# Performance work log

Hardware: AMD Instinct MI355X
Metric: run time of the kernel (lower is better)

The kernel has to match this reference:

```python
import jax, jax.numpy as jnp
import numpy as np

N_NODES = 100000
N_EDGES = 1600000
IN_DIM = 128
HID = 128
OUT = 128
NUM_GRAPHS = 2048


def setup_inputs() -> dict:
    key = jax.random.key(0)
    ks = jax.random.split(key, 10)
    x = jax.random.normal(ks[0], (N_NODES, IN_DIM), dtype=jnp.float32)
    edge_index = jax.random.randint(ks[1], (2, N_EDGES), 0, N_NODES, dtype=jnp.int32)
    graph_index = jnp.sort(jax.random.randint(ks[2], (N_NODES,), 0, NUM_GRAPHS, dtype=jnp.int32))
    def glorot(k, fi, fo):
        lim = jnp.sqrt(6.0 / (fi + fo)).astype(jnp.float32)
        return jax.random.uniform(k, (fi, fo), jnp.float32, -lim, lim)
    return {
        "x": x,
        "edge_index": edge_index,
        "graph_index": graph_index,
        "num_graphs": NUM_GRAPHS,
        "W1": glorot(ks[3], IN_DIM, HID), "b1": jnp.zeros((HID,), jnp.float32),
        "W2": glorot(ks[4], HID, HID),    "b2": jnp.zeros((HID,), jnp.float32),
        "W3": glorot(ks[5], HID, OUT),    "b3": jnp.zeros((OUT,), jnp.float32),
    }


def _gcn_layer(x, src, dst, norm, W, b, n_nodes):
    # transform first (cheap GEMM), then normalized gather-scatter aggregation
    h = x @ W                              # [N, F]
    msg = h[src] * norm[:, None]           # [E+N, F] gather + scale
    out = jax.ops.segment_sum(msg, dst, num_segments=n_nodes)  # scatter-add
    return out + b


def reference(x, edge_index, graph_index, num_graphs, W1, b1, W2, b2, W3, b3):
    n = x.shape[0]
    # add self-loops (PyG GCNConv default)
    loops = jnp.arange(n, dtype=edge_index.dtype)
    src = jnp.concatenate([edge_index[0], loops])
    dst = jnp.concatenate([edge_index[1], loops])
    # symmetric normalization D^-1/2 (A+I) D^-1/2, degree = in-degree incl. self-loop
    deg = jax.ops.segment_sum(jnp.ones_like(src, dtype=x.dtype), dst, num_segments=n)
    dinv = jax.lax.rsqrt(jnp.maximum(deg, 1.0))
    norm = dinv[src] * dinv[dst]
    # 3 conv layers + ReLU (dropout = identity at inference)
    h = jax.nn.relu(_gcn_layer(x, src, dst, norm, W1, b1, n))
    h = jax.nn.relu(_gcn_layer(h, src, dst, norm, W2, b2, n))
    h = jax.nn.relu(_gcn_layer(h, src, dst, norm, W3, b3, n))
    # global mean / max pooling per graph
    gsum = jax.ops.segment_sum(h, graph_index, num_segments=num_graphs)
    cnt = jax.ops.segment_sum(jnp.ones((n,), h.dtype), graph_index, num_segments=num_graphs)
    gmean = gsum / jnp.maximum(cnt, 1.0)[:, None]
    gmax = jax.ops.segment_max(h, graph_index, num_segments=num_graphs)
    return jnp.concatenate([gmean, gmax], axis=-1)
```

## Files before the change

### kernel.cpp

```cpp
#include <hip/hip_runtime.h>
#include <hip/hip_bf16.h>
#include <stdint.h>

#define N_NODES   100000
#define N_EDGES   1600000
#define FDIM      128
#define NUM_GR    2048
#define CSR_CAP   64

#define NBKT      391
#define BKT_CAP   4864
#define TILE      4096
#define LBIN_CAP  32
#define LBIN_STR  33

typedef __attribute__((ext_vector_type(8))) short short8;
typedef __attribute__((ext_vector_type(4))) float f32x4;

__device__ __forceinline__ uint32_t pk2(float a, float b) {
    __hip_bfloat16 x = __float2bfloat16(a), y = __float2bfloat16(b);
    uint16_t ux = *reinterpret_cast<uint16_t*>(&x);
    uint16_t uy = *reinterpret_cast<uint16_t*>(&y);
    return (uint32_t)ux | ((uint32_t)uy << 16);
}

__device__ __forceinline__ float bflo(uint32_t u) { return __uint_as_float(u << 16); }
__device__ __forceinline__ float bfhi(uint32_t u) { return __uint_as_float(u & 0xFFFF0000u); }


__global__ __launch_bounds__(256) void k_bucket_wprep(
        const int* __restrict__ src, const int* __restrict__ dst,
        int* __restrict__ bkt_cnt, int* __restrict__ bkt, int E, int gA,
        const float* __restrict__ W1, const float* __restrict__ W2,
        const float* __restrict__ W3, __hip_bfloat16* __restrict__ wt) {
    int b = blockIdx.x;
    if (b >= gA) {
        int idx = (b - gA) * 256 + threadIdx.x;
        int l = idx >> 14, rem = idx & 16383, c = rem >> 7, k = rem & 127;
        const float* W = (l == 0) ? W1 : ((l == 1) ? W2 : W3);
        wt[idx] = __float2bfloat16(W[k * FDIM + c]);
        return;
    }

    __shared__ int binCnt[NBKT];
    __shared__ int binBase[NBKT];
    __shared__ int bins[NBKT * LBIN_STR];

    for (int i = threadIdx.x; i < NBKT; i += 256) binCnt[i] = 0;
    __syncthreads();

    int e0 = b * TILE;
    int e1 = min(E, e0 + TILE);
    for (int e = e0 + threadIdx.x; e < e1; e += 256) {
        int s = src[e];
        int d = dst[e];
        int bi = d >> 8;
        int rec = ((d & 255) << 17) | s;
        int pos = atomicAdd(&binCnt[bi], 1);
        if (pos < LBIN_CAP) {
            bins[bi * LBIN_STR + pos] = rec;
        } else {
            int gp = atomicAdd(&bkt_cnt[bi], 1);
            if (gp < BKT_CAP) bkt[bi * BKT_CAP + gp] = rec;
        }
    }
    __syncthreads();

    for (int i = threadIdx.x; i < NBKT; i += 256) {
        int c = min(binCnt[i], LBIN_CAP);
        binBase[i] = (c > 0) ? atomicAdd(&bkt_cnt[i], c) : 0;
    }
    __syncthreads();

    for (int i = threadIdx.x; i < NBKT * LBIN_CAP; i += 256) {
        int bi = i / LBIN_CAP, sl = i - bi * LBIN_CAP;
        if (sl < min(binCnt[bi], LBIN_CAP)) {
            int gp = binBase[bi] + sl;
            if (gp < BKT_CAP) bkt[bi * BKT_CAP + gp] = bins[bi * LBIN_STR + sl];
        }
    }
}


__global__ __launch_bounds__(256) void k_csr(const int* __restrict__ bkt_cnt,
                                             const int* __restrict__ bkt,
                                             int* __restrict__ cnt,
                                             float* __restrict__ dinv,
                                             int* __restrict__ csr, int n) {
    __shared__ int lc[256];
    __shared__ int cur[256];
    int b = blockIdx.x;
    int tid = threadIdx.x;
    lc[tid] = 0;
    cur[tid] = 0;
    __syncthreads();

    int len = min(bkt_cnt[b], BKT_CAP);
    const int* recs = bkt + b * BKT_CAP;

    for (int i = tid; i < len; i += 256)
        atomicAdd(&lc[(recs[i] >> 17) & 255], 1);
    __syncthreads();

    int v = (b << 8) + tid;
    if (v < n) {
        int c = lc[tid];
        cnt[v] = c;
        dinv[v] = rsqrtf((float)(c + 1));
    }

    for (int i = tid; i < len; i += 256) {
        int rec = recs[i];
        int dl = (rec >> 17) & 255;
        int pos = atomicAdd(&cur[dl], 1);
        if (pos < CSR_CAP)
            csr[(((size_t)(b << 8) + dl) << 6) + pos] = rec & 0x1FFFF;
    }
}


template<bool AF32>
__global__ __launch_bounds__(256) void k_gemm(const void* __restrict__ Ap,
                                              const __hip_bfloat16* __restrict__ Wt,
                                              const float* __restrict__ dinv,
                                              __hip_bfloat16* __restrict__ C, int n) {
    __shared__ uint32_t lds[2 * 128 * 64];
    uint32_t* Atl = lds;
    uint32_t* Wtl = lds + 128 * 64;

    const int tid = threadIdx.x;
    const int rowBase = blockIdx.x * 128;

    if constexpr (AF32) {
        const float* A = (const float*)Ap;
        for (int it = 0; it < 16; ++it) {
            int g = it * 256 + tid;
            int r = g >> 5;
            int seg = g & 31;
            float4 v = make_float4(0.f, 0.f, 0.f, 0.f);
            if (rowBase + r < n) v = *(const float4*)&A[(size_t)(rowBase + r) * FDIM + seg * 4];
            int gg = seg >> 1;
            int word = r * 64 + (((gg ^ (r & 7)) << 2) | ((seg & 1) << 1));
            uint2 pv;
            pv.x = pk2(v.x, v.y);
            pv.y = pk2(v.z, v.w);
            *(uint2*)&Atl[word] = pv;
        }
    } else {
        const uint4* A4 = (const uint4*)Ap;
        for (int it = 0; it < 8; ++it) {
            int g = it * 256 + tid;
            int r = g >> 4;
            int seg = g & 15;
            uint4 v = make_uint4(0, 0, 0, 0);
            if (rowBase + r < n) v = A4[((size_t)rowBase + r) * 16 + seg];
            int word = r * 64 + ((seg ^ (r & 7)) << 2);
            *(uint4*)&Atl[word] = v;
        }
    }
    for (int it = 0; it < 8; ++it) {
        int g = it * 256 + tid;
        int r = g >> 4;
        int seg = g & 15;
        uint4 v = *(const uint4*)&Wt[(size_t)r * FDIM + seg * 8];
        int word = r * 64 + ((seg ^ (r & 7)) << 2);
        *(uint4*)&Wtl[word] = v;
    }
    __syncthreads();

    const int w = tid >> 6;
    const int lane = tid & 63;
    const int r = lane & 15;
    const int q = lane >> 4;

    f32x4 acc[8][2] = {};

#pragma unroll
    for (int kk = 0; kk < 4; ++kk) {
        int gr = ((kk * 4 + q) ^ (r & 7)) << 2;
        short8 a0 = *(const short8*)&Atl[(w * 32 + r) * 64 + gr];
        short8 a1 = *(const short8*)&Atl[(w * 32 + 16 + r) * 64 + gr];
#pragma unroll
        for (int m = 0; m < 8; ++m) {
            short8 bw = *(const short8*)&Wtl[(m * 16 + r) * 64 + gr];
            acc[m][0] = __builtin_amdgcn_mfma_f32_16x16x32_bf16(bw, a0, acc[m][0], 0, 0, 0);
            acc[m][1] = __builtin_amdgcn_mfma_f32_16x16x32_bf16(bw, a1, acc[m][1], 0, 0, 0);
        }
    }

#pragma unroll
    for (int nt = 0; nt < 2; ++nt) {
        int node = rowBase + w * 32 + nt * 16 + r;
        if (node < n) {
            float dv = dinv[node];
#pragma unroll
            for (int m = 0; m < 8; ++m) {
                f32x4 v = acc[m][nt];
                uint2 pv;
                pv.x = pk2(v[0] * dv, v[1] * dv);
                pv.y = pk2(v[2] * dv, v[3] * dv);
                *(uint2*)&C[(size_t)node * FDIM + m * 16 + q * 4] = pv;
            }
        }
    }
}


__global__ __launch_bounds__(256) void k_agg(const __hip_bfloat16* __restrict__ T,
                                             const int* __restrict__ cnt,
                                             const int* __restrict__ csr,
                                             const float* __restrict__ dinv,
                                             const float* __restrict__ bias,
                                             uint32_t* __restrict__ Hb,
                                             int n) {
    int wid = (blockIdx.x * 256 + threadIdx.x) >> 6;
    int lane = threadIdx.x & 63;
    if (wid >= n) return;
    int v = wid;
    int half = lane >> 5;
    int sub  = lane & 31;

    const uint2* Tu2 = (const uint2*)T;

    uint2 su = Tu2[(size_t)v * 32 + sub];
    float a0, a1, a2, a3;
    if (half == 0) { a0 = bflo(su.x); a1 = bfhi(su.x); a2 = bflo(su.y); a3 = bfhi(su.y); }
    else           { a0 = a1 = a2 = a3 = 0.f; }

    int cv = min(cnt[v], CSR_CAP);

    int sidx = (lane < cv) ? csr[((size_t)v << 6) + lane] : n;

    int mr = (cv + 15) & ~15;
    for (int j = 0; j < mr; j += 16) {
        uint2 gg[8];
#pragma unroll
        for (int t = 0; t < 8; ++t) {
            int it = __shfl(sidx, j + 2 * t + half, 64);
            gg[t] = Tu2[(size_t)it * 32 + sub];
        }
#pragma unroll
        for (int t = 0; t < 8; ++t) {
            a0 += bflo(gg[t].x);
            a1 += bfhi(gg[t].x);
            a2 += bflo(gg[t].y);
            a3 += bfhi(gg[t].y);
        }
    }

    float p0 = __shfl(a0, lane ^ 32, 64);
    float p1 = __shfl(a1, lane ^ 32, 64);
    float p2 = __shfl(a2, lane ^ 32, 64);
    float p3 = __shfl(a3, lane ^ 32, 64);
    a0 += p0; a1 += p1; a2 += p2; a3 += p3;

    if (half == 0) {
        float dv = dinv[v];
        float4 bb = *(const float4*)&bias[sub * 4];
        a0 = fmaxf(fmaf(dv, a0, bb.x), 0.f);
        a1 = fmaxf(fmaf(dv, a1, bb.y), 0.f);
        a2 = fmaxf(fmaf(dv, a2, bb.z), 0.f);
        a3 = fmaxf(fmaf(dv, a3, bb.w), 0.f);
        uint2 pv;
        pv.x = pk2(a0, a1);
        pv.y = pk2(a2, a3);
        *(uint2*)&Hb[(size_t)v * 64 + sub * 2] = pv;
    }
}


__device__ __forceinline__ int lower_bound_dev(const int* a, int n, int key) {
    int lo = 0, hi = n;
    while (lo < hi) {
        int m = (lo + hi) >> 1;
        if (a[m] < key) lo = m + 1; else hi = m;
    }
    return lo;
}

__global__ __launch_bounds__(64) void k_pool2(const uint32_t* __restrict__ Hb,
                                              const int* __restrict__ gidx,
                                              float* __restrict__ out, int n) {
    int g = blockIdx.x;
    int lane = threadIdx.x;

    int lo = lower_bound_dev(gidx, n, g);
    int hi = lower_bound_dev(gidx, n, g + 1);

    float s0 = 0.f, s1 = 0.f, m0 = 0.f, m1 = 0.f;
    for (int v = lo; v < hi; ++v) {
        uint32_t u = Hb[(size_t)v * 64 + lane];
        float x0 = bflo(u), x1 = bfhi(u);
        s0 += x0; s1 += x1;
        m0 = fmaxf(m0, x0); m1 = fmaxf(m1, x1);
    }
    float inv = 1.f / (float)max(hi - lo, 1);
    float* og = out + (size_t)g * 2 * FDIM;
    og[lane * 2]     = s0 * inv;
    og[lane * 2 + 1] = s1 * inv;
    og[FDIM + lane * 2]     = m0;
    og[FDIM + lane * 2 + 1] = m1;
}


extern "C" void kernel_launch(void* const* d_in, const int* in_sizes, int n_in,
                              void* d_out, int out_size, void* d_ws, size_t ws_size,
                              hipStream_t stream) {
    const float* x    = (const float*)d_in[0];
    const int*   ei   = (const int*)d_in[1];
    const int*   gidx = (const int*)d_in[2];
    const float* W1 = (const float*)d_in[4];
    const float* b1 = (const float*)d_in[5];
    const float* W2 = (const float*)d_in[6];
    const float* b2 = (const float*)d_in[7];
    const float* W3 = (const float*)d_in[8];
    const float* b3 = (const float*)d_in[9];
    float* out = (float*)d_out;

    const int N = N_NODES, E = N_EDGES;
    const int* src = ei;
    const int* dst = ei + E;

    char* ws = (char*)d_ws;
    size_t o = 0;
    auto alloc = [&](size_t bytes) { size_t r = o; o += (bytes + 255) & ~(size_t)255; return r; };
    size_t o_bktcnt = alloc((size_t)NBKT * 4);
    size_t o_bkt    = alloc((size_t)NBKT * BKT_CAP * 4);
    size_t o_cnt    = alloc((size_t)N * 4);
    size_t o_dinv   = alloc((size_t)N * 4);
    size_t o_csr    = alloc((size_t)NBKT * 256 * CSR_CAP * 4);
    size_t o_wt     = alloc((size_t)3 * FDIM * FDIM * 2);
    size_t o_t      = alloc((size_t)(N + 1) * FDIM * 2);
    size_t o_h      = alloc((size_t)N * FDIM * 2);

    int*   bkt_cnt = (int*)(ws + o_bktcnt);
    int*   bkt     = (int*)(ws + o_bkt);
    int*   cnt     = (int*)(ws + o_cnt);
    float* dinv    = (float*)(ws + o_dinv);
    int*   csr     = (int*)(ws + o_csr);
    __hip_bfloat16* wtbuf = (__hip_bfloat16*)(ws + o_wt);
    __hip_bfloat16* tbuf  = (__hip_bfloat16*)(ws + o_t);
    __hip_bfloat16* hb16  = (__hip_bfloat16*)(ws + o_h);

    hipMemsetAsync(bkt_cnt, 0, (size_t)NBKT * 4, stream);
    hipMemsetAsync(tbuf + (size_t)N * FDIM, 0, FDIM * 2, stream);

    const int gA = (E + TILE - 1) / TILE;

    k_bucket_wprep<<<gA + 192, 256, 0, stream>>>(src, dst, bkt_cnt, bkt, E, gA,
                                                 W1, W2, W3, wtbuf);
    k_csr<<<NBKT, 256, 0, stream>>>(bkt_cnt, bkt, cnt, dinv, csr, N);

    const int gGemm = (N + 127) / 128;
    const int gAgg  = (N + 3) / 4;

    k_gemm<true><<<gGemm, 256, 0, stream>>>(x, wtbuf, dinv, tbuf, N);
    k_agg<<<gAgg, 256, 0, stream>>>(tbuf, cnt, csr, dinv, b1, (uint32_t*)hb16, N);
    k_gemm<false><<<gGemm, 256, 0, stream>>>(hb16, wtbuf + FDIM * FDIM, dinv, tbuf, N);
    k_agg<<<gAgg, 256, 0, stream>>>(tbuf, cnt, csr, dinv, b2, (uint32_t*)hb16, N);
    k_gemm<false><<<gGemm, 256, 0, stream>>>(hb16, wtbuf + 2 * FDIM * FDIM, dinv, tbuf, N);
    k_agg<<<gAgg, 256, 0, stream>>>(tbuf, cnt, csr, dinv, b3, (uint32_t*)hb16, N);

    k_pool2<<<NUM_GR, 64, 0, stream>>>((const uint32_t*)hb16, gidx, out, N);
}
```

Baseline: 419.5 us.

## Slice transformed features into 8 column slabs so aggregation gathers stay cache-resident

```diff
diff --git a/kernel.cpp b/kernel.cpp
--- a/kernel.cpp
+++ b/kernel.cpp
@@ -13,6 +13,8 @@
 #define TILE      4096
 #define LBIN_CAP  32
 #define LBIN_STR  33
+
+#define NSLICE    8
 
 typedef __attribute__((ext_vector_type(8))) short short8;
 typedef __attribute__((ext_vector_type(4))) float f32x4;
@@ -86,11 +88,18 @@
                                              const int* __restrict__ bkt,
                                              int* __restrict__ cnt,
                                              float* __restrict__ dinv,
-                                             int* __restrict__ csr, int n) {
+                                             int* __restrict__ csr,
+                                             uint32_t* __restrict__ tz, int n) {
     __shared__ int lc[256];
     __shared__ int cur[256];
     int b = blockIdx.x;
     int tid = threadIdx.x;
+
+    if (b == 0 && tid < 64) {
+        int s = tid >> 3, wd = tid & 7;
+        tz[((size_t)s * (N_NODES + 1) + N_NODES) * 8 + wd] = 0;
+    }
+
     lc[tid] = 0;
     cur[tid] = 0;
     __syncthreads();
@@ -199,64 +208,75 @@
                 uint2 pv;
                 pv.x = pk2(v[0] * dv, v[1] * dv);
                 pv.y = pk2(v[2] * dv, v[3] * dv);
-                *(uint2*)&C[(size_t)node * FDIM + m * 16 + q * 4] = pv;
+                *(uint2*)&C[((size_t)m * (N_NODES + 1) + node) * 16 + q * 4] = pv;
             }
         }
     }
 }
 
 
-__global__ __launch_bounds__(256) void k_agg(const __hip_bfloat16* __restrict__ T,
+__global__ __launch_bounds__(256) void k_agg(const uint32_t* __restrict__ T,
                                              const int* __restrict__ cnt,
                                              const int* __restrict__ csr,
                                              const float* __restrict__ dinv,
                                              const float* __restrict__ bias,
                                              uint32_t* __restrict__ Hb,
                                              int n) {
-    int wid = (blockIdx.x * 256 + threadIdx.x) >> 6;
-    int lane = threadIdx.x & 63;
-    if (wid >= n) return;
-    int v = wid;
-    int half = lane >> 5;
-    int sub  = lane & 31;
-
-    const uint2* Tu2 = (const uint2*)T;
-
-    uint2 su = Tu2[(size_t)v * 32 + sub];
-    float a0, a1, a2, a3;
-    if (half == 0) { a0 = bflo(su.x); a1 = bfhi(su.x); a2 = bflo(su.y); a3 = bfhi(su.y); }
-    else           { a0 = a1 = a2 = a3 = 0.f; }
-
-    int cv = min(cnt[v], CSR_CAP);
-
-    int sidx = (lane < cv) ? csr[((size_t)v << 6) + lane] : n;
-
-    int mr = (cv + 15) & ~15;
-    for (int j = 0; j < mr; j += 16) {
-        uint2 gg[8];
-#pragma unroll
-        for (int t = 0; t < 8; ++t) {
-            int it = __shfl(sidx, j + 2 * t + half, 64);
-            gg[t] = Tu2[(size_t)it * 32 + sub];
-        }
-#pragma unroll
-        for (int t = 0; t < 8; ++t) {
-            a0 += bflo(gg[t].x);
-            a1 += bfhi(gg[t].x);
-            a2 += bflo(gg[t].y);
-            a3 += bfhi(gg[t].y);
-        }
-    }
-
-    float p0 = __shfl(a0, lane ^ 32, 64);
-    float p1 = __shfl(a1, lane ^ 32, 64);
-    float p2 = __shfl(a2, lane ^ 32, 64);
-    float p3 = __shfl(a3, lane ^ 32, 64);
-    a0 += p0; a1 += p1; a2 += p2; a3 += p3;
-
-    if (half == 0) {
+    const int sl    = blockIdx.x & 7;
+    const int chunk = blockIdx.x >> 3;
+    const int wave  = threadIdx.x >> 6;
+    const int lane  = threadIdx.x & 63;
+    const int g16   = lane >> 2;
+    const int q     = lane & 3;
+
+    const int v     = chunk * 64 + wave * 16 + g16;
+    const bool vv   = (v < n);
+    const int vsafe = vv ? v : 0;
+
+    int cg = 0;
+    if (vv) cg = min(__builtin_nontemporal_load(&cnt[v]), CSR_CAP);
+
+    int maxc = cg;
+    maxc = max(maxc, __shfl_xor(maxc, 4, 64));
+    maxc = max(maxc, __shfl_xor(maxc, 8, 64));
+    maxc = max(maxc, __shfl_xor(maxc, 16, 64));
+    maxc = max(maxc, __shfl_xor(maxc, 32, 64));
+
+    int val[16];
+#pragma unroll
+    for (int i = 0; i < 16; ++i) {
+        val[i] = n;
+        if (i * 4 < maxc)
+            val[i] = __builtin_nontemporal_load(&csr[((size_t)vsafe << 6) + i * 4 + q]);
+    }
+
+    const uint32_t* Ts = T + (size_t)sl * (N_NODES + 1) * 8;
+
+    float a0 = 0.f, a1 = 0.f, a2 = 0.f, a3 = 0.f;
+#pragma unroll
+    for (int i = 0; i < 16; ++i) {
+        if (i * 4 < maxc) {
+#pragma unroll
+            for (int jj = 0; jj < 4; ++jj) {
+                int j   = i * 4 + jj;
+                int bidx = __shfl(val[i], (g16 << 2) | jj, 64);
+                int idx = (j < cg) ? bidx : n;
+                uint2 uu = *(const uint2*)&Ts[(size_t)idx * 8 + q * 2];
+                a0 += bflo(uu.x); a1 += bfhi(uu.x);
+                a2 += bflo(uu.y); a3 += bfhi(uu.y);
+            }
+        }
+    }
+
+    {
+        uint2 su = *(const uint2*)&Ts[(size_t)vsafe * 8 + q * 2];
+        a0 += bflo(su.x); a1 += bfhi(su.x);
+        a2 += bflo(su.y); a3 += bfhi(su.y);
+    }
+
+    if (vv) {
         float dv = dinv[v];
-        float4 bb = *(const float4*)&bias[sub * 4];
+        float4 bb = *(const float4*)&bias[sl * 16 + q * 4];
         a0 = fmaxf(fmaf(dv, a0, bb.x), 0.f);
         a1 = fmaxf(fmaf(dv, a1, bb.y), 0.f);
         a2 = fmaxf(fmaf(dv, a2, bb.z), 0.f);
@@ -264,7 +284,9 @@
         uint2 pv;
         pv.x = pk2(a0, a1);
         pv.y = pk2(a2, a3);
-        *(uint2*)&Hb[(size_t)v * 64 + sub * 2] = pv;
+        unsigned long long ov = (unsigned long long)pv.x | ((unsigned long long)pv.y << 32);
+        __builtin_nontemporal_store(ov,
+            (unsigned long long*)&Hb[(size_t)v * 64 + sl * 8 + q * 2]);
     }
 }
 
@@ -343,23 +365,22 @@
     __hip_bfloat16* hb16  = (__hip_bfloat16*)(ws + o_h);
 
     hipMemsetAsync(bkt_cnt, 0, (size_t)NBKT * 4, stream);
-    hipMemsetAsync(tbuf + (size_t)N * FDIM, 0, FDIM * 2, stream);
 
     const int gA = (E + TILE - 1) / TILE;
 
     k_bucket_wprep<<<gA + 192, 256, 0, stream>>>(src, dst, bkt_cnt, bkt, E, gA,
                                                  W1, W2, W3, wtbuf);
-    k_csr<<<NBKT, 256, 0, stream>>>(bkt_cnt, bkt, cnt, dinv, csr, N);
+    k_csr<<<NBKT, 256, 0, stream>>>(bkt_cnt, bkt, cnt, dinv, csr, (uint32_t*)tbuf, N);
 
     const int gGemm = (N + 127) / 128;
-    const int gAgg  = (N + 3) / 4;
+    const int gAgg  = ((N + 63) / 64) * NSLICE;
 
     k_gemm<true><<<gGemm, 256, 0, stream>>>(x, wtbuf, dinv, tbuf, N);
-    k_agg<<<gAgg, 256, 0, stream>>>(tbuf, cnt, csr, dinv, b1, (uint32_t*)hb16, N);
+    k_agg<<<gAgg, 256, 0, stream>>>((const uint32_t*)tbuf, cnt, csr, dinv, b1, (uint32_t*)hb16, N);
     k_gemm<false><<<gGemm, 256, 0, stream>>>(hb16, wtbuf + FDIM * FDIM, dinv, tbuf, N);
-    k_agg<<<gAgg, 256, 0, stream>>>(tbuf, cnt, csr, dinv, b2, (uint32_t*)hb16, N);
+    k_agg<<<gAgg, 256, 0, stream>>>((const uint32_t*)tbuf, cnt, csr, dinv, b2, (uint32_t*)hb16, N);
     k_gemm<false><<<gGemm, 256, 0, stream>>>(hb16, wtbuf + 2 * FDIM * FDIM, dinv, tbuf, N);
-    k_agg<<<gAgg, 256, 0, stream>>>(tbuf, cnt, csr, dinv, b3, (uint32_t*)hb16, N);
+    k_agg<<<gAgg, 256, 0, stream>>>((const uint32_t*)tbuf, cnt, csr, dinv, b3, (uint32_t*)hb16, N);
 
     k_pool2<<<NUM_GR, 64, 0, stream>>>((const uint32_t*)hb16, gidx, out, N);
 }
```

Result: slower. 672.6 us (+60.3%).
